# Kernel optimization log

Hardware: AMD Instinct MI355X
Metric: run time of the kernel (lower is better)

The kernel has to match this reference:

```python
import jax, jax.numpy as jnp
import numpy as np

N_NODES = 200000
N_EDGES = 2000000
B = 1024
SEQ = 1000
EMB = 128
VOC = 26  # num_features_xt + 1
BN_EPS = 1e-5


def setup_inputs() -> dict:
    key = jax.random.key(0)
    ks = jax.random.split(key, 40)
    f32 = jnp.float32
    def nrm(k, shp, s=0.05):
        return jax.random.normal(k, shp, dtype=f32) * s
    inp = {}
    inp['x'] = jax.random.normal(ks[0], (N_NODES, 78), dtype=f32)
    inp['edge_index'] = jax.random.randint(ks[1], (2, N_EDGES), 0, N_NODES, dtype=jnp.int32)
    inp['batch'] = jnp.sort(jax.random.randint(ks[2], (N_NODES,), 0, B, dtype=jnp.int32))
    inp['target'] = jax.random.randint(ks[3], (B, SEQ), 0, VOC, dtype=jnp.int32)
    # GIN layer 1 (78 -> 32 -> 32)
    inp['W1a'] = nrm(ks[4], (78, 32)); inp['b1a'] = jnp.zeros((32,), f32)
    inp['W2a'] = nrm(ks[5], (32, 32)); inp['b2a'] = jnp.zeros((32,), f32)
    inp['g1'] = jnp.ones((32,), f32); inp['be1'] = jnp.zeros((32,), f32)
    # GIN layers 2-5 stacked
    inp['Ws1'] = nrm(ks[6], (4, 32, 32)); inp['bs1'] = jnp.zeros((4, 32), f32)
    inp['Ws2'] = nrm(ks[7], (4, 32, 32)); inp['bs2'] = jnp.zeros((4, 32), f32)
    inp['gs'] = jnp.ones((4, 32), f32); inp['bes'] = jnp.zeros((4, 32), f32)
    # drug head
    inp['fc1xd_W'] = nrm(ks[8], (32, 128)); inp['fc1xd_b'] = jnp.zeros((128,), f32)
    # protein branch
    inp['emb'] = nrm(ks[9], (VOC, EMB), 1.0)
    inp['convW'] = nrm(ks[10], (32, SEQ, 8))  # Conv1d(1000, 32, k=8): (O, I, K)
    inp['convb'] = jnp.zeros((32,), f32)
    inp['fcxt_W'] = nrm(ks[11], (32 * 121, 128)); inp['fcxt_b'] = jnp.zeros((128,), f32)
    # joint head
    inp['fc1_W'] = nrm(ks[12], (256, 1024)); inp['fc1_b'] = jnp.zeros((1024,), f32)
    inp['fc2_W'] = nrm(ks[13], (1024, 256)); inp['fc2_b'] = jnp.zeros((256,), f32)
    inp['out_W'] = nrm(ks[14], (256, 1)); inp['out_b'] = jnp.zeros((1,), f32)
    return inp


def _bn(h, g, b):
    m = h.mean(axis=0)
    v = h.var(axis=0)
    return (h - m) * jax.lax.rsqrt(v + BN_EPS) * g + b


def _gin(x, src, dst, W1, b1, W2, b2):
    # GIN aggregation (eps=0): (1+eps)*x + sum_{j->i} x_j, then 2-layer MLP
    agg = jax.ops.segment_sum(x[src], dst, num_segments=x.shape[0]) + x
    return jnp.maximum(agg @ W1 + b1, 0.0) @ W2 + b2


def reference(x, edge_index, batch, target, W1a, b1a, W2a, b2a, g1, be1,
              Ws1, bs1, Ws2, bs2, gs, bes, fc1xd_W, fc1xd_b, emb, convW, convb,
              fcxt_W, fcxt_b, fc1_W, fc1_b, fc2_W, fc2_b, out_W, out_b):
    relu = jax.nn.relu
    src, dst = edge_index[0], edge_index[1]
    h = _bn(relu(_gin(x, src, dst, W1a, b1a, W2a, b2a)), g1, be1)
    for i in range(4):
        h = _bn(relu(_gin(h, src, dst, Ws1[i], bs1[i], Ws2[i], bs2[i])), gs[i], bes[i])
    nb = target.shape[0]
    pooled = jax.ops.segment_sum(h, batch, num_segments=nb)  # [B, 32]
    xd = relu(pooled @ fc1xd_W + fc1xd_b)  # dropout: identity at eval
    # protein branch: embedding [B, 1000, 128] -> Conv1d over C=1000, L=128
    xe = emb[target]
    conv = jax.lax.conv_general_dilated(xe, convW, (1,), 'VALID',
                                        dimension_numbers=('NCH', 'OIH', 'NCH'))
    conv = conv + convb[None, :, None]  # [B, 32, 121]
    xt = conv.reshape(nb, 32 * 121) @ fcxt_W + fcxt_b
    xc = jnp.concatenate([xd, xt], axis=1)
    xc = relu(xc @ fc1_W + fc1_b)
    xc = relu(xc @ fc2_W + fc2_b)
    return xc @ out_W + out_b
```

## Files before the change

kernel.cpp:

```cpp
#include <hip/hip_runtime.h>

#define N_NODES 200000
#define N_EDGES 2000000
#define BATCH   1024
#define SEQ     1000
#define EMBD    128
#define VOC     26
#define BN_EPS  1e-5f
#define NB      128
#define NBUK    1563
#define CAP     1664
#define CH0     896
#define CH1     768
#define STG     4096
#define BPT     7



__global__ __launch_bounds__(256, 2) void k_bscatter(const int* __restrict__ ei,
                                                     int* __restrict__ gcnt,
                                                     unsigned int* __restrict__ epk) {
    __shared__ int lcnt[NBUK];
    __shared__ int lpos[NBUK];
    __shared__ int sbase[NBUK];
    __shared__ int ssum[256];
    __shared__ int2 stage[STG];
    int tid = threadIdx.x;
    int e0 = blockIdx.x * STG;
    int m = min(STG, N_EDGES - e0);
    for (int i = tid; i < NBUK; i += 256) lcnt[i] = 0;
    __syncthreads();
    for (int i = tid; i < m; i += 256) {
        int d = ei[N_EDGES + e0 + i];
        atomicAdd(&lcnt[d >> 7], 1);
    }
    __syncthreads();
    int v[BPT]; int s0 = 0; int bb = tid * BPT;
#pragma unroll
    for (int k = 0; k < BPT; k++) {
        int idx = bb + k;
        v[k] = (idx < NBUK) ? lcnt[idx] : 0;
        s0 += v[k];
    }
    ssum[tid] = s0;
    __syncthreads();
    for (int off = 1; off < 256; off <<= 1) {
        int x = (tid >= off) ? ssum[tid - off] : 0;
        __syncthreads();
        ssum[tid] += x;
        __syncthreads();
    }
    int run = ssum[tid] - s0;
#pragma unroll
    for (int k = 0; k < BPT; k++) {
        int idx = bb + k;
        if (idx < NBUK) { lpos[idx] = run; run += v[k]; }
    }
    __syncthreads();
    for (int i = tid; i < NBUK; i += 256) {
        int c = lcnt[i];
        if (c > 0) {
            int gb = atomicAdd(&gcnt[i], c);
            sbase[i] = gb - lpos[i];
        }
    }
    __syncthreads();
    for (int i = tid; i < m; i += 256) {
        int s = ei[e0 + i];
        int d = ei[N_EDGES + e0 + i];
        int p = atomicAdd(&lpos[d >> 7], 1);
        stage[p] = make_int2(s, d);
    }
    __syncthreads();
    for (int i = tid; i < m; i += 256) {
        int2 ed = stage[i];
        int b = ed.y >> 7;
        int slot = sbase[b] + i;
        if (slot < CAP)
            epk[(size_t)b * CAP + slot] = ((unsigned int)ed.x << 8) | (unsigned int)(ed.y & 127);
    }
}

__global__ __launch_bounds__(256, 8) void k_bsort(const int* __restrict__ gcnt,
                                                  unsigned int* __restrict__ epk,
                                                  int* __restrict__ deg) {
    __shared__ unsigned int stg[CAP];
    __shared__ unsigned int srt[CAP];
    __shared__ int cnt[NB];
    __shared__ int pos[NB];
    int b = blockIdx.x, tid = threadIdx.x;
    int fill = min(gcnt[b], CAP);
    unsigned int* slab = epk + (size_t)b * CAP;
    for (int i = tid; i < fill; i += 256) stg[i] = slab[i];
    if (tid < NB) cnt[tid] = 0;
    __syncthreads();
    for (int i = tid; i < fill; i += 256) atomicAdd(&cnt[stg[i] & (NB - 1)], 1);
    __syncthreads();
    if (tid < NB) { pos[tid] = cnt[tid]; deg[b * NB + tid] = cnt[tid]; }
    __syncthreads();
    for (int off = 1; off < NB; off <<= 1) {
        int x = (tid < NB && tid >= off) ? pos[tid - off] : 0;
        __syncthreads();
        if (tid < NB) pos[tid] += x;
        __syncthreads();
    }
    if (tid < NB) cnt[tid] = pos[tid] - cnt[tid];
    __syncthreads();
    for (int i = tid; i < fill; i += 256) {
        int p = atomicAdd(&cnt[stg[i] & (NB - 1)], 1);
        srt[p] = stg[i];
    }
    __syncthreads();
    for (int i = tid; i < fill; i += 256) slab[i] = srt[i];
}


__global__ __launch_bounds__(128) void k_proj78(const float* __restrict__ x,
                                                const float* __restrict__ W,
                                                float* __restrict__ y) {
    __shared__ __align__(16) float xs[128 * 78];
    __shared__ __align__(16) float ws[78 * 32];
    int tid = threadIdx.x;
    int base = blockIdx.x * 128;
    for (int i = tid; i < 78 * 32; i += 128) ws[i] = W[i];
    int cnt = min(128, N_NODES - base);
    for (int i = tid; i < cnt * 78; i += 128) xs[i] = x[(size_t)base * 78 + i];
    __syncthreads();
    int n = base + tid;
    if (tid >= cnt) return;
    float acc[32];
#pragma unroll
    for (int j = 0; j < 32; j++) acc[j] = 0.f;
    const float* xr = &xs[tid * 78];
    for (int c = 0; c < 78; c++) {
        float xv = xr[c];
        const float4* w4 = (const float4*)&ws[c * 32];
#pragma unroll
        for (int j4 = 0; j4 < 8; j4++) {
            float4 w = w4[j4];
            acc[j4 * 4 + 0] += xv * w.x; acc[j4 * 4 + 1] += xv * w.y;
            acc[j4 * 4 + 2] += xv * w.z; acc[j4 * 4 + 3] += xv * w.w;
        }
    }
    float4* yo = (float4*)&y[(size_t)n * 32];
#pragma unroll
    for (int j4 = 0; j4 < 8; j4++)
        yo[j4] = make_float4(acc[j4*4], acc[j4*4+1], acc[j4*4+2], acc[j4*4+3]);
}

template <bool FOLD>
__global__ __launch_bounds__(256, 7) void k_gmlp(const float* __restrict__ hin,
                                                 const int* __restrict__ gcnt,
                                                 const unsigned int* __restrict__ epk,
                                                 const int* __restrict__ deg,
                                                 const float* __restrict__ stats,
                                                 const float* __restrict__ g,
                                                 const float* __restrict__ be,
                                                 const float* __restrict__ W1,
                                                 const float* __restrict__ b1,
                                                 const float* __restrict__ W2,
                                                 const float* __restrict__ b2,
                                                 float* __restrict__ h,
                                                 float* __restrict__ statsOut) {
    __shared__ __align__(16) float ts[129 * 33];
    __shared__ __align__(16) unsigned int es[CH0];
    __shared__ float b1s[32], b2s[32], as_[32], cs_[32], cv[32];
    int tid = threadIdx.x, base = blockIdx.x * NB;
    if (tid < 32) { b1s[tid] = b1[tid]; b2s[tid] = b2[tid]; }
    int cnt = min(NB, N_NODES - base);
    int fill = min(gcnt[blockIdx.x], CAP);
    int dg = 0;
    if (FOLD && tid < cnt) dg = deg[base + tid];
    if constexpr (FOLD) {
        if (tid < 32) {
            float inv_n = 1.f / (float)N_NODES;
            float m = stats[tid] * inv_n;
            float var = stats[32 + tid] * inv_n - m * m;
            float a = g[tid] * rsqrtf(var + BN_EPS);
            as_[tid] = a;
            cs_[tid] = be[tid] - m * a;
        }
    }
    for (int i = tid; i < cnt * 32; i += 256) ts[(i >> 5) * 33 + (i & 31)] = hin[(size_t)base * 32 + i];
    if constexpr (FOLD) {
        __syncthreads();
        if (tid < 32) {
            float s = 0.f;
            for (int k = 0; k < 32; k++) s += cs_[k] * W1[k * 32 + tid];
            cv[tid] = s;
        }
    }
    {
        int hw = tid >> 5, c = tid & 31;
        const unsigned int* slab = epk + (size_t)blockIdx.x * CAP;
#pragma unroll
        for (int ch = 0; ch < 2; ch++) {
            int cbase = ch ? CH0 : 0;
            int clen  = ch ? CH1 : CH0;
            __syncthreads();
            for (int i = tid; i < clen; i += 256) {
                int gi = cbase + i;
                es[i] = (gi < fill) ? slab[gi] : 128u;
            }
            __syncthreads();
            for (int se = hw * 16; se < clen; se += 128) {
                float rr[16]; int dd[16];
#pragma unroll
                for (int k = 0; k < 16; k++) {
                    unsigned int p = es[se + k];
                    rr[k] = hin[(size_t)(p >> 8) * 32 + c];
                    dd[k] = (int)(p & 255u);
                }
                float acc = rr[0]; int cur = dd[0];
#pragma unroll
                for (int k = 1; k < 16; k++) {
                    if (dd[k] == cur) acc += rr[k];
                    else { atomicAdd(&ts[cur * 33 + c], acc); acc = rr[k]; cur = dd[k]; }
                }
                if (cur < 128) atomicAdd(&ts[cur * 33 + c], acc);
            }
        }
    }
    __syncthreads();
    float* spq = (float*)es;
    float t[32];
    if (tid < cnt) {
        float v[32];
        if constexpr (FOLD) {
            float dgf = (float)(dg + 1);
#pragma unroll
            for (int j = 0; j < 32; j++) v[j] = b1s[j] + dgf * cv[j];
            for (int c = 0; c < 32; c++) {
                float avs = ts[tid * 33 + c] * as_[c];
                const float4* w4 = (const float4*)&W1[c * 32];
#pragma unroll
                for (int j4 = 0; j4 < 8; j4++) {
                    float4 w = w4[j4];
                    v[j4*4+0] += avs * w.x; v[j4*4+1] += avs * w.y;
                    v[j4*4+2] += avs * w.z; v[j4*4+3] += avs * w.w;
                }
            }
        } else {
#pragma unroll
            for (int c = 0; c < 32; c++) v[c] = ts[tid * 33 + c] + b1s[c];
        }
        float acc[32];
#pragma unroll
        for (int j = 0; j < 32; j++) acc[j] = b2s[j];
        for (int c = 0; c < 32; c++) {
            float zv = fmaxf(v[c], 0.f);
            const float4* w4 = (const float4*)&W2[c * 32];
#pragma unroll
            for (int j4 = 0; j4 < 8; j4++) {
                float4 w = w4[j4];
                acc[j4*4+0] += zv * w.x; acc[j4*4+1] += zv * w.y;
                acc[j4*4+2] += zv * w.z; acc[j4*4+3] += zv * w.w;
            }
        }
#pragma unroll
        for (int j = 0; j < 32; j++) t[j] = fmaxf(acc[j], 0.f);
    } else {
#pragma unroll
        for (int j = 0; j < 32; j++) t[j] = 0.f;
    }
    __syncthreads();
    if (tid < NB) {
#pragma unroll
        for (int c = 0; c < 32; c++) ts[tid * 33 + c] = t[c];
    }
    __syncthreads();
    {
        int c = tid & 31, gg = tid >> 5;
        float s = 0.f, q = 0.f;
        for (int r = gg * 16; r < gg * 16 + 16; r++) { float vv = ts[r * 33 + c]; s += vv; q += vv * vv; }
        spq[gg * 32 + c] = s; spq[256 + gg * 32 + c] = q;
    }
    __syncthreads();
    if (tid < 32) {
        float s = 0.f, q = 0.f;
#pragma unroll
        for (int gg = 0; gg < 8; gg++) { s += spq[gg * 32 + tid]; q += spq[256 + gg * 32 + tid]; }
        atomicAdd(&statsOut[tid], s);
        atomicAdd(&statsOut[32 + tid], q);
    }
    for (int i = tid; i < cnt * 32; i += 256) h[(size_t)base * 32 + i] = ts[(i >> 5) * 33 + (i & 31)];
}

__device__ __forceinline__ int lbound(const int* __restrict__ b, int val) {
    int lo = 0, hi = N_NODES;
    while (lo < hi) { int mid = (lo + hi) >> 1; if (b[mid] < val) lo = mid + 1; else hi = mid; }
    return lo;
}

__global__ __launch_bounds__(256) void k_pool(const float* __restrict__ h,
                                              const int* __restrict__ batch,
                                              const float* __restrict__ stats,
                                              const float* __restrict__ gw,
                                              const float* __restrict__ be,
                                              float* __restrict__ pooled) {
    __shared__ float sp[8][32];
    int g = blockIdx.x;
    int start = lbound(batch, g), end = lbound(batch, g + 1);
    int c = threadIdx.x & 31, gg = threadIdx.x >> 5;
    float acc = 0.f;
    for (int r = start + gg; r < end; r += 8) acc += h[(size_t)r * 32 + c];
    sp[gg][c] = acc;
    __syncthreads();
    if (threadIdx.x < 32) {
        int j = threadIdx.x;
        float s = 0.f;
#pragma unroll
        for (int k = 0; k < 8; k++) s += sp[k][j];
        float inv_n = 1.f / (float)N_NODES;
        float m = stats[j] * inv_n;
        float var = stats[32 + j] * inv_n - m * m;
        float a = gw[j] * rsqrtf(var + BN_EPS);
        float cc = be[j] - m * a;
        pooled[g * 32 + j] = a * s + cc * (float)(end - start);
    }
}

__global__ __launch_bounds__(256) void k_xd(const float* __restrict__ pooled,
                                            const float* __restrict__ W,
                                            const float* __restrict__ b,
                                            float* __restrict__ xc) {
    int t = blockIdx.x * 256 + threadIdx.x;
    int row = t >> 7, col = t & 127;
    if (row >= BATCH) return;
    float acc = b[col];
    for (int k = 0; k < 32; k++) acc += pooled[row * 32 + k] * W[k * 128 + col];
    xc[row * 256 + col] = fmaxf(acc, 0.f);
}


__global__ __launch_bounds__(256) void k_trw(const float* __restrict__ convW,
                                             float* __restrict__ Wt) {
    int t = blockIdx.x * 256 + threadIdx.x;
    if (t >= 32 * SEQ * 8) return;
    int o = t / (SEQ * 8), r = t % (SEQ * 8), i = r >> 3, k = r & 7;
    Wt[i * 256 + o * 8 + k] = convW[t];
}

__global__ __launch_bounds__(256) void k_prot1(const int* __restrict__ target,
                                               const float* __restrict__ Wt,
                                               float* __restrict__ Sg) {
    __shared__ int tv[SEQ];
    __shared__ int pos_[SEQ];
    __shared__ int off_[VOC + 1];
    __shared__ int cur_[VOC];
    int tid = threadIdx.x, b = blockIdx.x;
    for (int i = tid; i < SEQ; i += 256) tv[i] = target[(size_t)b * SEQ + i];
    if (tid < VOC + 1) off_[tid] = 0;
    __syncthreads();
    for (int i = tid; i < SEQ; i += 256) atomicAdd(&off_[tv[i] + 1], 1);
    __syncthreads();
    if (tid == 0) for (int v = 1; v <= VOC; v++) off_[v] += off_[v - 1];
    __syncthreads();
    if (tid < VOC) cur_[tid] = off_[tid];
    __syncthreads();
    for (int i = tid; i < SEQ; i += 256) {
        int p = atomicAdd(&cur_[tv[i]], 1);
        pos_[p] = i;
    }
    __syncthreads();
    for (int v = 0; v < VOC; v++) {
        int e0 = off_[v], e1 = off_[v + 1];
        float a0 = 0.f, a1 = 0.f, a2 = 0.f, a3 = 0.f, a4 = 0.f, a5 = 0.f, a6 = 0.f, a7 = 0.f;
        int k = e0;
        for (; k + 8 <= e1; k += 8) {
            a0 += Wt[(size_t)pos_[k + 0] * 256 + tid];
            a1 += Wt[(size_t)pos_[k + 1] * 256 + tid];
            a2 += Wt[(size_t)pos_[k + 2] * 256 + tid];
            a3 += Wt[(size_t)pos_[k + 3] * 256 + tid];
            a4 += Wt[(size_t)pos_[k + 4] * 256 + tid];
            a5 += Wt[(size_t)pos_[k + 5] * 256 + tid];
            a6 += Wt[(size_t)pos_[k + 6] * 256 + tid];
            a7 += Wt[(size_t)pos_[k + 7] * 256 + tid];
        }
        for (; k < e1; k++) a0 += Wt[(size_t)pos_[k] * 256 + tid];
        Sg[((size_t)b * VOC + v) * 256 + tid] = ((a0 + a1) + (a2 + a3)) + ((a4 + a5) + (a6 + a7));
    }
}

__global__ __launch_bounds__(256, 4) void k_prot2(const float* __restrict__ Sg,
                                                  const float* __restrict__ emb,
                                                  const float* __restrict__ convb,
                                                  float* __restrict__ conv) {
    __shared__ __align__(16) float S[VOC * 256];
    __shared__ __align__(16) float embs[VOC * EMBD];
    int tid = threadIdx.x, b = blockIdx.x;
    for (int i = tid; i < VOC * 256; i += 256) S[i] = Sg[(size_t)b * (VOC * 256) + i];
    for (int i = tid; i < VOC * EMBD; i += 256) embs[i] = emb[i];
    __syncthreads();
    int og = tid >> 6, lt = tid & 63;
    bool has2 = (lt < 57);
    float acc0[8], acc1[8];
#pragma unroll
    for (int oi = 0; oi < 8; oi++) {
        float bb = convb[og * 8 + oi];
        acc0[oi] = bb; acc1[oi] = bb;
    }
    for (int v = 0; v < VOC; v++) {
        float er0[8], er1[8];
#pragma unroll
        for (int k = 0; k < 8; k++) er0[k] = embs[v * EMBD + lt + k];
#pragma unroll
        for (int k = 0; k < 8; k++) er1[k] = has2 ? embs[v * EMBD + lt + 64 + k] : 0.f;
        const float* sv = &S[v * 256 + og * 64];
#pragma unroll
        for (int oi = 0; oi < 8; oi++) {
#pragma unroll
            for (int k = 0; k < 8; k++) {
                float s = sv[oi * 8 + k];
                acc0[oi] += s * er0[k];
                acc1[oi] += s * er1[k];
            }
        }
    }
#pragma unroll
    for (int oi = 0; oi < 8; oi++) {
        int o = og * 8 + oi;
        conv[((size_t)b * 32 + o) * 121 + lt] = acc0[oi];
        if (has2) conv[((size_t)b * 32 + o) * 121 + lt + 64] = acc1[oi];
    }
}


__global__ __launch_bounds__(256) void k_init_bias(float* __restrict__ C, int ldc, int coff,
                                                   const float* __restrict__ bias, int nb) {
    int t = blockIdx.x * 256 + threadIdx.x;
    int row = t / nb, col = t % nb;
    if (row >= BATCH) return;
    C[row * ldc + coff + col] = bias[col];
}

template <int ROWS, bool ATOMIC, bool RELU>
__global__ __launch_bounds__(256, 3) void k_gemm(const float* __restrict__ A, int lda,
                                                 const float* __restrict__ W, int ldw,
                                                 const float* __restrict__ bias,
                                                 float* __restrict__ C, int ldc, int coff,
                                                 int mtc, int ntc, int klen) {
    constexpr int P  = ROWS + 4;
    constexpr int HR = ROWS / 2;
    constexpr int TPR = 256 / ROWS;
    __shared__ __align__(16) float As[64 * P];
    __shared__ __align__(16) float Ws[64 * 128];
    int bid = blockIdx.x;
    int mt = bid % mtc, nt = (bid / mtc) % ntc, ks = bid / (mtc * ntc);
    int row0 = mt * ROWS, col0 = nt * 128, k0 = ks * klen;
    int tid = threadIdx.x;
    int j = tid & 127, rh = tid >> 7;
    float acc[HR];
#pragma unroll
    for (int m = 0; m < HR; m++) acc[m] = (ATOMIC || bias == nullptr) ? 0.f : bias[col0 + j];
    int lr = tid / TPR, lk = tid % TPR;
    for (int kc = 0; kc < klen; kc += 64) {
        int cc = min(64, klen - kc);
        __syncthreads();
        for (int kk = lk; kk < cc; kk += TPR)
            As[kk * P + lr] = A[(size_t)(row0 + lr) * lda + k0 + kc + kk];
        for (int i = tid; i < cc * 32; i += 256) {
            int r = i >> 5, c4 = (i & 31) << 2;
            *(float4*)&Ws[r * 128 + c4] =
                *(const float4*)&W[(size_t)(k0 + kc + r) * ldw + col0 + c4];
        }
        __syncthreads();
#pragma unroll 4
        for (int kk = 0; kk < cc; kk++) {
            float w = Ws[kk * 128 + j];
            const float4* a4 = (const float4*)&As[kk * P + rh * HR];
#pragma unroll
            for (int m4 = 0; m4 < HR / 4; m4++) {
                float4 a = a4[m4];
                acc[m4*4+0] += a.x * w; acc[m4*4+1] += a.y * w;
                acc[m4*4+2] += a.z * w; acc[m4*4+3] += a.w * w;
            }
        }
    }
#pragma unroll
    for (int m = 0; m < HR; m++) {
        int row = row0 + rh * HR + m;
        float* p = &C[(size_t)row * ldc + coff + col0 + j];
        if (ATOMIC) atomicAdd(p, acc[m]);
        else { float v = acc[m]; if (RELU) v = fmaxf(v, 0.f); *p = v; }
    }
}

__global__ __launch_bounds__(256) void k_out(const float* __restrict__ xc2,
                                             const float* __restrict__ W,
                                             const float* __restrict__ b,
                                             float* __restrict__ out) {
    int gt = blockIdx.x * 256 + threadIdx.x;
    int wid = gt >> 6, lane = gt & 63;
    if (wid >= BATCH) return;
    float4 xv = ((const float4*)&xc2[(size_t)wid * 256])[lane];
    float4 wv = ((const float4*)W)[lane];
    float s = fmaxf(xv.x, 0.f) * wv.x + fmaxf(xv.y, 0.f) * wv.y +
              fmaxf(xv.z, 0.f) * wv.z + fmaxf(xv.w, 0.f) * wv.w;
    for (int off = 32; off; off >>= 1) s += __shfl_down(s, off, 64);
    if (lane == 0) out[wid] = s + b[0];
}


extern "C" void kernel_launch(void* const* d_in, const int* in_sizes, int n_in,
                              void* d_out, int out_size, void* d_ws, size_t ws_size,
                              hipStream_t stream) {
    const float* x      = (const float*)d_in[0];
    const int*   ei     = (const int*)d_in[1];
    const int*   batch  = (const int*)d_in[2];
    const int*   target = (const int*)d_in[3];
    const float* W1a = (const float*)d_in[4];
    const float* b1a = (const float*)d_in[5];
    const float* W2a = (const float*)d_in[6];
    const float* b2a = (const float*)d_in[7];
    const float* g1  = (const float*)d_in[8];
    const float* be1 = (const float*)d_in[9];
    const float* Ws1 = (const float*)d_in[10];
    const float* bs1 = (const float*)d_in[11];
    const float* Ws2 = (const float*)d_in[12];
    const float* bs2 = (const float*)d_in[13];
    const float* gs  = (const float*)d_in[14];
    const float* bes = (const float*)d_in[15];
    const float* fc1xd_W = (const float*)d_in[16];
    const float* fc1xd_b = (const float*)d_in[17];
    const float* emb   = (const float*)d_in[18];
    const float* convW = (const float*)d_in[19];
    const float* convb = (const float*)d_in[20];
    const float* fcxt_W = (const float*)d_in[21];
    const float* fcxt_b = (const float*)d_in[22];
    const float* fc1_W = (const float*)d_in[23];
    const float* fc1_b = (const float*)d_in[24];
    const float* fc2_W = (const float*)d_in[25];
    const float* fc2_b = (const float*)d_in[26];
    const float* out_W = (const float*)d_in[27];
    const float* out_b = (const float*)d_in[28];
    float* out = (float*)d_out;

    char* ws = (char*)d_ws;
    size_t off = 0;
    auto alloc = [&](size_t bytes) { char* p = ws + off; off += (bytes + 4095) & ~(size_t)4095; return p; };
    float* y    = (float*)alloc((size_t)N_NODES * 32 * 4);
    float* h    = (float*)alloc((size_t)N_NODES * 32 * 4);
    unsigned int* epk = (unsigned int*)alloc((size_t)NBUK * CAP * 4);
    int* gcnt = (int*)alloc((size_t)NBUK * 4);
    float* stats  = (float*)alloc(5 * 64 * 4);
    float* pooled = (float*)alloc(BATCH * 32 * 4);
    float* xc  = (float*)alloc(BATCH * 256 * 4);
    float* xc1 = (float*)alloc(BATCH * 1024 * 4);
    float* xc2 = (float*)alloc(BATCH * 256 * 4);
    float* Wt  = (float*)alloc(SEQ * 256 * 4);
    int* deg  = (int*)alloc((size_t)NBUK * NB * 4);
    float* Sg   = h;
    float* conv = y;

    hipMemsetAsync(stats, 0, 5 * 64 * 4, stream);
    hipMemsetAsync(gcnt, 0, (size_t)NBUK * 4, stream);

    const int PROJ78_G = (N_NODES + 127) / 128;
    const int PART_G   = (N_EDGES + STG - 1) / STG;

    k_bscatter<<<PART_G, 256, 0, stream>>>(ei, gcnt, epk);
    k_bsort<<<NBUK, 256, 0, stream>>>(gcnt, epk, deg);

    k_proj78<<<PROJ78_G, 128, 0, stream>>>(x, W1a, y);
    k_gmlp<false><<<NBUK, 256, 0, stream>>>(y, gcnt, epk, deg, nullptr, nullptr, nullptr,
                                            nullptr, b1a, W2a, b2a, h, stats);
    float* hin = h; float* hout = y;
    for (int i = 0; i < 4; i++) {
        const float* gg = (i == 0) ? g1 : gs + (i - 1) * 32;
        const float* bb = (i == 0) ? be1 : bes + (i - 1) * 32;
        k_gmlp<true><<<NBUK, 256, 0, stream>>>(hin, gcnt, epk, deg, stats + i * 64, gg, bb,
                                               Ws1 + i * 1024, bs1 + i * 32, Ws2 + i * 1024,
                                               bs2 + i * 32, hout, stats + (i + 1) * 64);
        float* tmp = hin; hin = hout; hout = tmp;
    }
    k_pool<<<BATCH, 256, 0, stream>>>(hin, batch, stats + 4 * 64, gs + 3 * 32, bes + 3 * 32, pooled);
    k_xd<<<(BATCH * 128) / 256, 256, 0, stream>>>(pooled, fc1xd_W, fc1xd_b, xc);
    k_trw<<<(32 * SEQ * 8) / 256, 256, 0, stream>>>(convW, Wt);
    k_prot1<<<BATCH, 256, 0, stream>>>(target, Wt, Sg);
    k_prot2<<<BATCH, 256, 0, stream>>>(Sg, emb, convb, conv);
    k_init_bias<<<(BATCH * 128) / 256, 256, 0, stream>>>(xc, 256, 128, fcxt_b, 128);
    k_gemm<32, true, false><<<32 * 1 * 16, 256, 0, stream>>>(conv, 3872, fcxt_W, 128, nullptr,
                                                             xc, 256, 128, 32, 1, 242);
    k_gemm<32, false, true><<<32 * 8 * 1, 256, 0, stream>>>(xc, 256, fc1_W, 1024, fc1_b,
                                                            xc1, 1024, 0, 32, 8, 256);
    k_init_bias<<<(BATCH * 256) / 256, 256, 0, stream>>>(xc2, 256, 0, fc2_b, 256);
    k_gemm<32, true, false><<<32 * 2 * 4, 256, 0, stream>>>(xc1, 1024, fc2_W, 256, nullptr,
                                                            xc2, 256, 0, 32, 2, 256);
    k_out<<<(BATCH * 64) / 256, 256, 0, stream>>>(xc2, out_W, out_b, out);
}
```

Baseline: 1.016 ms.

## Fuse graph pooling into last GIN layer and widen GIN blocks to 512 threads

The last GIN layer now accumulates per-graph raw sums and node counts directly via atomics instead of writing h and running a separate pooling kernel. BatchNorm is applied afterwards inside k_xd using the final stats. The GIN kernel also moves to 512 threads, loads the whole edge slab (CAP raised to 1792) into shared memory at once instead of in two chunks, and drops a barrier. The aim is to save a full-size h write/read and a binary-search pool kernel, and to get more parallelism during the edge gather, at the cost of more atomics and more shared memory per block.

```diff
diff --git a/kernel.cpp b/kernel.cpp
--- a/kernel.cpp
+++ b/kernel.cpp
@@ -9,9 +9,7 @@
 #define BN_EPS  1e-5f
 #define NB      128
 #define NBUK    1563
-#define CAP     1664
-#define CH0     896
-#define CH1     768
+#define CAP     1792
 #define STG     4096
 #define BPT     7
 
@@ -148,8 +146,8 @@
         yo[j4] = make_float4(acc[j4*4], acc[j4*4+1], acc[j4*4+2], acc[j4*4+3]);
 }
 
-template <bool FOLD>
-__global__ __launch_bounds__(256, 7) void k_gmlp(const float* __restrict__ hin,
+template <bool FOLD, bool POOL>
+__global__ __launch_bounds__(512, 8) void k_gmlp(const float* __restrict__ hin,
                                                  const int* __restrict__ gcnt,
                                                  const unsigned int* __restrict__ epk,
                                                  const int* __restrict__ deg,
@@ -161,14 +159,19 @@
                                                  const float* __restrict__ W2,
                                                  const float* __restrict__ b2,
                                                  float* __restrict__ h,
-                                                 float* __restrict__ statsOut) {
+                                                 float* __restrict__ statsOut,
+                                                 const int* __restrict__ batch,
+                                                 float* __restrict__ praw,
+                                                 int* __restrict__ pcnt) {
     __shared__ __align__(16) float ts[129 * 33];
-    __shared__ __align__(16) unsigned int es[CH0];
+    __shared__ __align__(16) unsigned int es[CAP];
     __shared__ float b1s[32], b2s[32], as_[32], cs_[32], cv[32];
+    __shared__ int bts[NB];
     int tid = threadIdx.x, base = blockIdx.x * NB;
     if (tid < 32) { b1s[tid] = b1[tid]; b2s[tid] = b2[tid]; }
     int cnt = min(NB, N_NODES - base);
     int fill = min(gcnt[blockIdx.x], CAP);
+    int pfill = (fill + 255) & ~255;
     int dg = 0;
     if (FOLD && tid < cnt) dg = deg[base + tid];
     if constexpr (FOLD) {
@@ -181,9 +184,15 @@
             cs_[tid] = be[tid] - m * a;
         }
     }
-    for (int i = tid; i < cnt * 32; i += 256) ts[(i >> 5) * 33 + (i & 31)] = hin[(size_t)base * 32 + i];
+    if constexpr (POOL) {
+        for (int i = tid; i < cnt; i += 512) bts[i] = batch[base + i];
+    }
+    const unsigned int* slab = epk + (size_t)blockIdx.x * CAP;
+    for (int i = tid; i < fill; i += 512) es[i] = slab[i];
+    for (int i = fill + tid; i < pfill; i += 512) es[i] = 128u;
+    for (int i = tid; i < cnt * 32; i += 512) ts[(i >> 5) * 33 + (i & 31)] = hin[(size_t)base * 32 + i];
+    __syncthreads();
     if constexpr (FOLD) {
-        __syncthreads();
         if (tid < 32) {
             float s = 0.f;
             for (int k = 0; k < 32; k++) s += cs_[k] * W1[k * 32 + tid];
@@ -192,33 +201,21 @@
     }
     {
         int hw = tid >> 5, c = tid & 31;
-        const unsigned int* slab = epk + (size_t)blockIdx.x * CAP;
-#pragma unroll
-        for (int ch = 0; ch < 2; ch++) {
-            int cbase = ch ? CH0 : 0;
-            int clen  = ch ? CH1 : CH0;
-            __syncthreads();
-            for (int i = tid; i < clen; i += 256) {
-                int gi = cbase + i;
-                es[i] = (gi < fill) ? slab[gi] : 128u;
+        for (int se = hw * 16; se < pfill; se += 256) {
+            float rr[16]; int dd[16];
+#pragma unroll
+            for (int k = 0; k < 16; k++) {
+                unsigned int p = es[se + k];
+                rr[k] = hin[(size_t)(p >> 8) * 32 + c];
+                dd[k] = (int)(p & 255u);
             }
-            __syncthreads();
-            for (int se = hw * 16; se < clen; se += 128) {
-                float rr[16]; int dd[16];
-#pragma unroll
-                for (int k = 0; k < 16; k++) {
-                    unsigned int p = es[se + k];
-                    rr[k] = hin[(size_t)(p >> 8) * 32 + c];
-                    dd[k] = (int)(p & 255u);
-                }
-                float acc = rr[0]; int cur = dd[0];
-#pragma unroll
-                for (int k = 1; k < 16; k++) {
-                    if (dd[k] == cur) acc += rr[k];
-                    else { atomicAdd(&ts[cur * 33 + c], acc); acc = rr[k]; cur = dd[k]; }
-                }
-                if (cur < 128) atomicAdd(&ts[cur * 33 + c], acc);
+            float acc = rr[0]; int cur = dd[0];
+#pragma unroll
+            for (int k = 1; k < 16; k++) {
+                if (dd[k] == cur) acc += rr[k];
+                else { atomicAdd(&ts[cur * 33 + c], acc); acc = rr[k]; cur = dd[k]; }
             }
+            if (cur < 128) atomicAdd(&ts[cur * 33 + c], acc);
         }
     }
     __syncthreads();
@@ -259,17 +256,19 @@
         }
 #pragma unroll
         for (int j = 0; j < 32; j++) t[j] = fmaxf(acc[j], 0.f);
-    } else {
-#pragma unroll
-        for (int j = 0; j < 32; j++) t[j] = 0.f;
     }
     __syncthreads();
     if (tid < NB) {
-#pragma unroll
-        for (int c = 0; c < 32; c++) ts[tid * 33 + c] = t[c];
-    }
-    __syncthreads();
-    {
+        if (tid < cnt) {
+#pragma unroll
+            for (int c = 0; c < 32; c++) ts[tid * 33 + c] = t[c];
+        } else {
+#pragma unroll
+            for (int c = 0; c < 32; c++) ts[tid * 33 + c] = 0.f;
+        }
+    }
+    __syncthreads();
+    if (tid < 256) {
         int c = tid & 31, gg = tid >> 5;
         float s = 0.f, q = 0.f;
         for (int r = gg * 16; r < gg * 16 + 16; r++) { float vv = ts[r * 33 + c]; s += vv; q += vv * vv; }
@@ -283,52 +282,54 @@
         atomicAdd(&statsOut[tid], s);
         atomicAdd(&statsOut[32 + tid], q);
     }
-    for (int i = tid; i < cnt * 32; i += 256) h[(size_t)base * 32 + i] = ts[(i >> 5) * 33 + (i & 31)];
-}
-
-__device__ __forceinline__ int lbound(const int* __restrict__ b, int val) {
-    int lo = 0, hi = N_NODES;
-    while (lo < hi) { int mid = (lo + hi) >> 1; if (b[mid] < val) lo = mid + 1; else hi = mid; }
-    return lo;
-}
-
-__global__ __launch_bounds__(256) void k_pool(const float* __restrict__ h,
-                                              const int* __restrict__ batch,
-                                              const float* __restrict__ stats,
-                                              const float* __restrict__ gw,
-                                              const float* __restrict__ be,
-                                              float* __restrict__ pooled) {
-    __shared__ float sp[8][32];
-    int g = blockIdx.x;
-    int start = lbound(batch, g), end = lbound(batch, g + 1);
-    int c = threadIdx.x & 31, gg = threadIdx.x >> 5;
-    float acc = 0.f;
-    for (int r = start + gg; r < end; r += 8) acc += h[(size_t)r * 32 + c];
-    sp[gg][c] = acc;
-    __syncthreads();
-    if (threadIdx.x < 32) {
-        int j = threadIdx.x;
-        float s = 0.f;
-#pragma unroll
-        for (int k = 0; k < 8; k++) s += sp[k][j];
-        float inv_n = 1.f / (float)N_NODES;
-        float m = stats[j] * inv_n;
-        float var = stats[32 + j] * inv_n - m * m;
-        float a = gw[j] * rsqrtf(var + BN_EPS);
-        float cc = be[j] - m * a;
-        pooled[g * 32 + j] = a * s + cc * (float)(end - start);
-    }
-}
-
-__global__ __launch_bounds__(256) void k_xd(const float* __restrict__ pooled,
+    if constexpr (POOL) {
+        if (tid < 32) {
+            int c = tid;
+            float s = 0.f; int curg = bts[0]; int rc = 0;
+            for (int r = 0; r < cnt; r++) {
+                int gb = bts[r];
+                if (gb != curg) {
+                    atomicAdd(&praw[curg * 32 + c], s);
+                    if (c == 0) atomicAdd(&pcnt[curg], rc);
+                    s = 0.f; rc = 0; curg = gb;
+                }
+                s += ts[r * 33 + c]; rc++;
+            }
+            atomicAdd(&praw[curg * 32 + c], s);
+            if (c == 0) atomicAdd(&pcnt[curg], rc);
+        }
+    } else {
+        for (int i = tid; i < cnt * 32; i += 512) h[(size_t)base * 32 + i] = ts[(i >> 5) * 33 + (i & 31)];
+    }
+}
+
+__global__ __launch_bounds__(256) void k_xd(const float* __restrict__ praw,
+                                            const int* __restrict__ pcnt,
+                                            const float* __restrict__ stats,
+                                            const float* __restrict__ gw,
+                                            const float* __restrict__ bev,
                                             const float* __restrict__ W,
                                             const float* __restrict__ b,
                                             float* __restrict__ xc) {
-    int t = blockIdx.x * 256 + threadIdx.x;
+    __shared__ float a_[32], c_[32];
+    int tid = threadIdx.x;
+    if (tid < 32) {
+        float inv_n = 1.f / (float)N_NODES;
+        float m = stats[tid] * inv_n;
+        float var = stats[32 + tid] * inv_n - m * m;
+        float a = gw[tid] * rsqrtf(var + BN_EPS);
+        a_[tid] = a; c_[tid] = bev[tid] - m * a;
+    }
+    __syncthreads();
+    int t = blockIdx.x * 256 + tid;
     int row = t >> 7, col = t & 127;
     if (row >= BATCH) return;
+    float cntf = (float)pcnt[row];
     float acc = b[col];
-    for (int k = 0; k < 32; k++) acc += pooled[row * 32 + k] * W[k * 128 + col];
+    for (int k = 0; k < 32; k++) {
+        float p = a_[k] * praw[row * 32 + k] + c_[k] * cntf;
+        acc += p * W[k * 128 + col];
+    }
     xc[row * 256 + col] = fmaxf(acc, 0.f);
 }
 
@@ -544,7 +545,8 @@
     unsigned int* epk = (unsigned int*)alloc((size_t)NBUK * CAP * 4);
     int* gcnt = (int*)alloc((size_t)NBUK * 4);
     float* stats  = (float*)alloc(5 * 64 * 4);
-    float* pooled = (float*)alloc(BATCH * 32 * 4);
+    float* praw   = (float*)alloc(BATCH * 32 * 4);
+    int*   pcnt   = (int*)alloc(BATCH * 4);
     float* xc  = (float*)alloc(BATCH * 256 * 4);
     float* xc1 = (float*)alloc(BATCH * 1024 * 4);
     float* xc2 = (float*)alloc(BATCH * 256 * 4);
@@ -555,6 +557,8 @@
 
     hipMemsetAsync(stats, 0, 5 * 64 * 4, stream);
     hipMemsetAsync(gcnt, 0, (size_t)NBUK * 4, stream);
+    hipMemsetAsync(praw, 0, BATCH * 32 * 4, stream);
+    hipMemsetAsync(pcnt, 0, BATCH * 4, stream);
 
     const int PROJ78_G = (N_NODES + 127) / 128;
     const int PART_G   = (N_EDGES + STG - 1) / STG;
@@ -563,19 +567,26 @@
     k_bsort<<<NBUK, 256, 0, stream>>>(gcnt, epk, deg);
 
     k_proj78<<<PROJ78_G, 128, 0, stream>>>(x, W1a, y);
-    k_gmlp<false><<<NBUK, 256, 0, stream>>>(y, gcnt, epk, deg, nullptr, nullptr, nullptr,
-                                            nullptr, b1a, W2a, b2a, h, stats);
+    k_gmlp<false, false><<<NBUK, 512, 0, stream>>>(y, gcnt, epk, deg, nullptr, nullptr, nullptr,
+                                                   nullptr, b1a, W2a, b2a, h, stats,
+                                                   nullptr, nullptr, nullptr);
     float* hin = h; float* hout = y;
-    for (int i = 0; i < 4; i++) {
+    for (int i = 0; i < 3; i++) {
         const float* gg = (i == 0) ? g1 : gs + (i - 1) * 32;
         const float* bb = (i == 0) ? be1 : bes + (i - 1) * 32;
-        k_gmlp<true><<<NBUK, 256, 0, stream>>>(hin, gcnt, epk, deg, stats + i * 64, gg, bb,
-                                               Ws1 + i * 1024, bs1 + i * 32, Ws2 + i * 1024,
-                                               bs2 + i * 32, hout, stats + (i + 1) * 64);
+        k_gmlp<true, false><<<NBUK, 512, 0, stream>>>(hin, gcnt, epk, deg, stats + i * 64, gg, bb,
+                                                      Ws1 + i * 1024, bs1 + i * 32, Ws2 + i * 1024,
+                                                      bs2 + i * 32, hout, stats + (i + 1) * 64,
+                                                      nullptr, nullptr, nullptr);
         float* tmp = hin; hin = hout; hout = tmp;
     }
-    k_pool<<<BATCH, 256, 0, stream>>>(hin, batch, stats + 4 * 64, gs + 3 * 32, bes + 3 * 32, pooled);
-    k_xd<<<(BATCH * 128) / 256, 256, 0, stream>>>(pooled, fc1xd_W, fc1xd_b, xc);
+    k_gmlp<true, true><<<NBUK, 512, 0, stream>>>(hin, gcnt, epk, deg, stats + 3 * 64,
+                                                 gs + 2 * 32, bes + 2 * 32,
+                                                 Ws1 + 3 * 1024, bs1 + 3 * 32, Ws2 + 3 * 1024,
+                                                 bs2 + 3 * 32, hout, stats + 4 * 64,
+                                                 batch, praw, pcnt);
+    k_xd<<<(BATCH * 128) / 256, 256, 0, stream>>>(praw, pcnt, stats + 4 * 64,
+                                                  gs + 3 * 32, bes + 3 * 32, fc1xd_W, fc1xd_b, xc);
     k_trw<<<(32 * SEQ * 8) / 256, 256, 0, stream>>>(convW, Wt);
     k_prot1<<<BATCH, 256, 0, stream>>>(target, Wt, Sg);
     k_prot2<<<BATCH, 256, 0, stream>>>(Sg, emb, convb, conv);
```

New measurement: 1.077 ms. +6.0%, slower.
